# Optimization experiments

Measured on AMD Instinct MI355X. Metric: run time of the kernel, lower is better.

The kernel has to match this reference:

```python
import jax, jax.numpy as jnp
import numpy as np
import math

B = 50        # graphs per batch
NPG = 2000    # nodes per graph
EPG = 12000   # edges per graph
F_IN = 256
NHID = 128
RATIO = 0.8


def setup_inputs() -> dict:
    key = jax.random.key(0)
    ks = jax.random.split(key, 12)
    N = B * NPG
    src_loc = jax.random.randint(ks[0], (B, EPG), 0, NPG)
    dst_loc = jax.random.randint(ks[1], (B, EPG), 0, NPG)
    off = (jnp.arange(B) * NPG)[:, None]
    edge_index = jnp.stack([(src_loc + off).reshape(-1), (dst_loc + off).reshape(-1)]).astype(jnp.int32)

    def lin(k, fi, fo):
        return (jax.random.normal(k, (fi, fo), jnp.float32) / np.sqrt(fi).astype(np.float32))

    return {
        "x": jax.random.normal(ks[2], (N, F_IN), jnp.float32),
        "W1": lin(ks[3], F_IN, NHID), "b1": jnp.zeros(NHID, jnp.float32),
        "Ws1": lin(ks[4], NHID, 1), "bs1": jnp.zeros(1, jnp.float32),
        "W2": lin(ks[5], NHID, NHID), "b2": jnp.zeros(NHID, jnp.float32),
        "Ws2": lin(ks[6], NHID, 1), "bs2": jnp.zeros(1, jnp.float32),
        "W3": lin(ks[7], NHID, NHID), "b3": jnp.zeros(NHID, jnp.float32),
        "Ws3": lin(ks[8], NHID, 1), "bs3": jnp.zeros(1, jnp.float32),
        "Wl": lin(ks[9], 2 * NHID, NHID), "bl": jnp.zeros(NHID, jnp.float32),
        "edge_index": edge_index,
    }


def gcn_conv(x, W, b, src, dst, w, N):
    # PyG GCNConv: D^{-1/2} (A + I) D^{-1/2} X W + b, deg from edge weights + self loop
    h = x @ W
    deg = jax.ops.segment_sum(w, dst, num_segments=N) + 1.0
    dis = jax.lax.rsqrt(deg)
    norm = w * dis[src] * dis[dst]                       # [E]
    agg = jax.ops.segment_sum(h[src] * norm[:, None], dst, num_segments=N)
    return agg + h / deg[:, None] + b                    # self-loop norm = 1/deg


def sag_pool(x, src, dst, w, Ws, bs, n_per_graph):
    N = x.shape[0]
    k = math.ceil(RATIO * n_per_graph)
    score = gcn_conv(x, Ws, bs, src, dst, w, N)[:, 0]    # [N]
    _, topi = jax.lax.top_k(score.reshape(B, n_per_graph), k)
    perm = (topi + (jnp.arange(B) * n_per_graph)[:, None]).reshape(-1)
    x_new = x[perm] * jnp.tanh(score[perm])[:, None]
    # filter_adj: keep edges whose endpoints survive, reindex; dropped edges -> weight 0
    mapping = jnp.full((N,), -1, jnp.int32).at[perm].set(jnp.arange(B * k, dtype=jnp.int32))
    ns, nd = mapping[src], mapping[dst]
    valid = (ns >= 0) & (nd >= 0) & (w > 0)
    return (x_new, jnp.where(valid, ns, 0), jnp.where(valid, nd, 0),
            jnp.where(valid, w, jnp.zeros((), x.dtype)), k)


def readout(x, n):
    # global max pool || global mean pool (equal-size graphs, nodes grouped per graph)
    xr = x.reshape(B, n, -1)
    return jnp.concatenate([xr.max(axis=1), xr.mean(axis=1)], axis=-1)


def reference(x, W1, b1, Ws1, bs1, W2, b2, Ws2, bs2, W3, b3, Ws3, bs3, Wl, bl, edge_index):
    src, dst = edge_index[0], edge_index[1]
    w = jnp.ones(src.shape[0], x.dtype)
    n = NPG
    x = jax.nn.relu(gcn_conv(x, W1, b1, src, dst, w, B * n))
    x, src, dst, w, n = sag_pool(x, src, dst, w, Ws1, bs1, n)
    x1 = readout(x, n)
    x = jax.nn.relu(gcn_conv(x, W2, b2, src, dst, w, B * n))
    x, src, dst, w, n = sag_pool(x, src, dst, w, Ws2, bs2, n)
    x2 = readout(x, n)
    x = jax.nn.relu(gcn_conv(x, W3, b3, src, dst, w, B * n))
    x, src, dst, w, n = sag_pool(x, src, dst, w, Ws3, bs3, n)
    x3 = readout(x, n)
    return jax.nn.relu((x1 + x2 + x3) @ Wl + bl)
```

## Files before the change

kernel.cpp:

```cpp
#include <hip/hip_runtime.h>
#include <math.h>

#define B_GRAPHS 50
#define NPG0     2000
#define EPG      12000
#define F_IN_C   256
#define NHID     128
#define N0       (B_GRAPHS * NPG0)
#define NE       (B_GRAPHS * EPG)
#define RSEG     32
#define GSLOTS   7
#define CPAD     136
#define KMAX     1600

typedef _Float16 f16x8 __attribute__((ext_vector_type(8)));
typedef float    f32x4 __attribute__((ext_vector_type(4)));

static inline int cdiv(int a, int b) { return (a + b - 1) / b; }

__global__ void k_fill_start(int* __restrict__ cnt, float* __restrict__ accum) {
    int i = blockIdx.x * 256 + threadIdx.x;
    if (i < N0) cnt[i] = 0;
    if (i < B_GRAPHS * 256) accum[i] = 0.f;
}

__global__ void k_init_cvt(const int* __restrict__ ei, int* __restrict__ esrc,
                           int* __restrict__ edst, float* __restrict__ ew,
                           int* __restrict__ cnt,
                           const float* __restrict__ W1, const float* __restrict__ W2,
                           const float* __restrict__ W3, _Float16* __restrict__ WT1,
                           _Float16* __restrict__ WT2, _Float16* __restrict__ WT3) {
    int t = blockIdx.x * 256 + threadIdx.x;
    if (t < NE) {
        int d = ei[NE + t];
        esrc[t] = ei[t]; edst[t] = d; ew[t] = 1.0f;
        atomicAdd(&cnt[d], 1);
    }
    if (t < 128 * 256) {
        int n = t >> 8, kk = t & 255;
        WT1[t] = (_Float16)W1[kk * 128 + n];
    } else if (t < 128 * 256 + 128 * 128) {
        int u = t - 32768; int n = u >> 7, kk = u & 127;
        WT2[u] = (_Float16)W2[kk * 128 + n];
    } else if (t < 128 * 256 + 2 * 128 * 128) {
        int u = t - 49152; int n = u >> 7, kk = u & 127;
        WT3[u] = (_Float16)W3[kk * 128 + n];
    }
}

template<int FP32IN, int F, int GATHER>
__global__ __launch_bounds__(256) void k_gemm_ws(const void* __restrict__ Xin,
                                                 const _Float16* __restrict__ WT,
                                                 const int* __restrict__ perm,
                                                 const float* __restrict__ gate,
                                                 _Float16* __restrict__ H, int N) {
    constexpr int KH  = (F > 128) ? 128 : F;
    constexpr int K8H = KH / 8;
    constexpr int SMEMSZ = (128 * KH > 64 * CPAD) ? 128 * KH : 64 * CPAD;
    __shared__ _Float16 smem[SMEMSZ];
    const int tid  = threadIdx.x;
    const int wave = tid >> 6, lane = tid & 63;
    const int quad = lane >> 4, l16 = lane & 15;
    const int m_blk = blockIdx.x * 64;

    f32x4 acc[8];
#pragma unroll
    for (int j = 0; j < 8; ++j) acc[j] = {0.f, 0.f, 0.f, 0.f};

    int row0 = m_blk + wave * 16 + l16;
    if (row0 > N - 1) row0 = N - 1;
    _Float16 g0 = (_Float16)1.0f;
    if (GATHER) {
        g0 = (_Float16)gate[row0];
        row0 = perm[row0];
    }
    const int sx = l16 & 7;
    constexpr int NKQ = F / 32;

    if (FP32IN) {
        constexpr int PD = (NKQ < 4) ? NKQ : 4;
        const float* base0 = (const float*)Xin + (size_t)row0 * F + quad * 8;
        float4 p0[PD][2];
#pragma unroll
        for (int i = 0; i < PD; ++i) {
            p0[i][0] = ((const float4*)(base0 + i * 32))[0];
            p0[i][1] = ((const float4*)(base0 + i * 32))[1];
        }
#pragma unroll
        for (int c = tid; c < 128 * K8H; c += 256) {
            int n = c / K8H, k8 = c - n * K8H;
            f16x8 v = *(const f16x8*)&WT[(size_t)(n * (F / 8) + k8) * 8];
            *(f16x8*)&smem[n * KH + ((k8 ^ (n & 7)) << 3)] = v;
        }
        __syncthreads();
#pragma unroll
        for (int kq = 0; kq < NKQ; ++kq) {
            if (KH < F && kq == NKQ / 2) {
                __syncthreads();
#pragma unroll
                for (int c = tid; c < 128 * K8H; c += 256) {
                    int n = c / K8H, k8 = c - n * K8H;
                    f16x8 v = *(const f16x8*)&WT[(size_t)(n * (F / 8) + K8H + k8) * 8];
                    *(f16x8*)&smem[n * KH + ((k8 ^ (n & 7)) << 3)] = v;
                }
                __syncthreads();
            }
            const int b = kq % PD;
            float4 f0 = p0[b][0], f1 = p0[b][1];
            if (kq + PD < NKQ) {
                p0[b][0] = ((const float4*)(base0 + (kq + PD) * 32))[0];
                p0[b][1] = ((const float4*)(base0 + (kq + PD) * 32))[1];
            }
            f16x8 af0 = (f16x8){(_Float16)f0.x,(_Float16)f0.y,(_Float16)f0.z,(_Float16)f0.w,
                                (_Float16)f1.x,(_Float16)f1.y,(_Float16)f1.z,(_Float16)f1.w};
            f16x8 bf[8];
#pragma unroll
            for (int j = 0; j < 8; ++j)
                bf[j] = *(const f16x8*)&smem[(j * 16 + l16) * KH + (((((kq & 3) << 2) + quad) ^ sx) << 3)];
#pragma unroll
            for (int j = 0; j < 8; ++j)
                acc[j] = __builtin_amdgcn_mfma_f32_16x16x32_f16(af0, bf[j], acc[j], 0, 0, 0);
        }
    } else {
#pragma unroll
        for (int c = tid; c < 128 * K8H; c += 256) {
            int n = c / K8H, k8 = c - n * K8H;
            f16x8 v = *(const f16x8*)&WT[(size_t)(n * K8H + k8) * 8];
            *(f16x8*)&smem[n * KH + ((k8 ^ (n & 7)) << 3)] = v;
        }
        const _Float16* base0 = (const _Float16*)Xin + (size_t)row0 * F + quad * 8;
        f16x8 q0[NKQ];
#pragma unroll
        for (int i = 0; i < NKQ; ++i)
            q0[i] = *(const f16x8*)(base0 + i * 32);
        __syncthreads();
#pragma unroll
        for (int kq = 0; kq < NKQ; ++kq) {
            f16x8 af0 = q0[kq];
            if (GATHER) af0 = af0 * g0;
            f16x8 bf[8];
#pragma unroll
            for (int j = 0; j < 8; ++j)
                bf[j] = *(const f16x8*)&smem[(j * 16 + l16) * KH + (((((kq & 3) << 2) + quad) ^ sx) << 3)];
#pragma unroll
            for (int j = 0; j < 8; ++j)
                acc[j] = __builtin_amdgcn_mfma_f32_16x16x32_f16(af0, bf[j], acc[j], 0, 0, 0);
        }
    }
    __syncthreads();

    _Float16* sC = smem;
    const int rw = wave * 16;
#pragma unroll
    for (int j = 0; j < 8; ++j)
#pragma unroll
        for (int g = 0; g < 4; ++g)
            sC[(rw + quad * 4 + g) * CPAD + j * 16 + l16] = (_Float16)acc[j][g];
    __syncthreads();
    {
        int rr = tid >> 2;
        int cc = (tid & 3) * 32;
        int gr = m_blk + rr;
        if (gr < N) {
            _Float16* Hr = H + (size_t)gr * 128 + cc;
            const _Float16* Sr = sC + rr * CPAD + cc;
#pragma unroll
            for (int c = 0; c < 4; ++c)
                *(f16x8*)&Hr[c * 8] = *(const f16x8*)&Sr[c * 8];
        }
    }
}

__global__ __launch_bounds__(1024) void k_scancsr(const int* __restrict__ cnt,
                                                  int* __restrict__ offs,
                                                  const int* __restrict__ esrc,
                                                  const int* __restrict__ edst,
                                                  const float* __restrict__ ew,
                                                  int* __restrict__ csr_src,
                                                  float* __restrict__ csr_norm,
                                                  int npg) {
    __shared__ int ch[1024];
    __shared__ int scnt[2048];
    __shared__ int scur[2048];
    int b = blockIdx.x, tid = threadIdx.x;
    int base = b * npg;
    int per = (npg + 1023) >> 10;
    int s0 = tid * per;
    int s1 = s0 + per; if (s1 > npg) s1 = npg; if (s0 > npg) s0 = npg;
    int s = 0;
    for (int i = s0; i < s1; ++i) { int c = cnt[base + i]; scnt[i] = c; s += c; }
    ch[tid] = s;
    __syncthreads();
    for (int d = 1; d < 1024; d <<= 1) {
        int t = ch[tid] + ((tid >= d) ? ch[tid - d] : 0);
        __syncthreads();
        ch[tid] = t;
        __syncthreads();
    }
    int run = b * EPG + ch[tid] - s;
    for (int i = s0; i < s1; ++i) {
        offs[base + i] = run; scur[i] = run;
        run += scnt[i];
    }
    __syncthreads();
    int e0 = b * EPG;
    for (int e = tid; e < EPG; e += 1024) {
        float w = ew[e0 + e];
        if (w > 0.f) {
            int sN = esrc[e0 + e], d = edst[e0 + e];
            int pos = atomicAdd(&scur[d - base], 1);
            csr_src[pos] = sN;
            csr_norm[pos] = rsqrtf((float)(scnt[sN - base] + 1)) *
                            rsqrtf((float)(scnt[d - base] + 1));
        }
    }
}

__global__ __launch_bounds__(256) void k_agg(const _Float16* __restrict__ H,
                                             const int* __restrict__ csr_src,
                                             const float* __restrict__ csr_norm,
                                             const int* __restrict__ offs,
                                             const int* __restrict__ cnt,
                                             const float* __restrict__ bias,
                                             const float* __restrict__ Ws,
                                             _Float16* __restrict__ X,
                                             float* __restrict__ hs,
                                             int bpg, int npg) {
    int bi = blockIdx.x;
    int x = bi & 7, s = bi >> 3;
    int gslot = s / bpg, blk = s - gslot * bpg;
    int g = x + 8 * gslot;
    if (g >= B_GRAPHS) return;
    int node = g * npg + blk * 4 + (threadIdx.x >> 6);
    int lane = threadIdx.x & 63;
    int quad = lane >> 4, l16 = lane & 15;

    int st = offs[node], c = cnt[node], en = st + c;
    float acc[8];
#pragma unroll
    for (int j = 0; j < 8; ++j) acc[j] = 0.f;

    if (c > 0) {
        for (int e0 = st; e0 < en; e0 += 8) {
            int eA = e0 + quad, eB = eA + 4;
            int ecA = eA < en ? eA : en - 1;
            int ecB = eB < en ? eB : en - 1;
            int uA = csr_src[ecA], uB = csr_src[ecB];
            float nA = (eA < en) ? csr_norm[ecA] : 0.f;
            float nB = (eB < en) ? csr_norm[ecB] : 0.f;
            f16x8 hA = *(const f16x8*)&H[(size_t)uA * NHID + l16 * 8];
            f16x8 hB = *(const f16x8*)&H[(size_t)uB * NHID + l16 * 8];
#pragma unroll
            for (int j = 0; j < 8; ++j) acc[j] = fmaf((float)hA[j], nA, acc[j]);
#pragma unroll
            for (int j = 0; j < 8; ++j) acc[j] = fmaf((float)hB[j], nB, acc[j]);
        }
    }
#pragma unroll
    for (int j = 0; j < 8; ++j) {
        acc[j] += __shfl_xor(acc[j], 16, 64);
        acc[j] += __shfl_xor(acc[j], 32, 64);
    }
    float invd = 1.f / (float)(c + 1);
    f16x8 hn = *(const f16x8*)&H[(size_t)node * NHID + l16 * 8];
    float4 b0 = *(const float4*)&bias[l16 * 8];
    float4 b1 = *(const float4*)&bias[l16 * 8 + 4];
    float4 w0 = *(const float4*)&Ws[l16 * 8];
    float4 w1 = *(const float4*)&Ws[l16 * 8 + 4];
    const float bb[8] = {b0.x, b0.y, b0.z, b0.w, b1.x, b1.y, b1.z, b1.w};
    const float ww[8] = {w0.x, w0.y, w0.z, w0.w, w1.x, w1.y, w1.z, w1.w};
    float sd = 0.f;
    f16x8 o;
#pragma unroll
    for (int j = 0; j < 8; ++j) {
        float v = fmaxf(acc[j] + (float)hn[j] * invd + bb[j], 0.f);
        o[j] = (_Float16)v;
        sd = fmaf(v, ww[j], sd);
    }
    if (quad == 0)
        *(f16x8*)&X[(size_t)node * NHID + l16 * 8] = o;
    sd += __shfl_xor(sd, 1, 64);
    sd += __shfl_xor(sd, 2, 64);
    sd += __shfl_xor(sd, 4, 64);
    sd += __shfl_xor(sd, 8, 64);
    if (lane == 0) hs[node] = sd;
}

template<int REMAP, int COMB>
__global__ __launch_bounds__(1024) void k_scoretopk(const float* __restrict__ hs,
                                                    int* __restrict__ csr_src,
                                                    float* __restrict__ csr_norm,
                                                    int* __restrict__ offs,
                                                    const int* __restrict__ cnt,
                                                    const float* __restrict__ bs,
                                                    int* __restrict__ perm,
                                                    float* __restrict__ gate,
                                                    int* __restrict__ esrc,
                                                    int* __restrict__ edst,
                                                    float* __restrict__ ew,
                                                    int* __restrict__ cntN,
                                                    const float* __restrict__ pmax,
                                                    const float* __restrict__ psum,
                                                    float* __restrict__ accum,
                                                    int npg, int k) {
    __shared__ float ss[2048];
    __shared__ int   si[2048];
    __shared__ float shs[2048];
    __shared__ int   shist[KMAX];
    int b = blockIdx.x, tid = threadIdx.x;
    int base = b * npg;

    if (COMB) {
        if (tid < 2 * NHID) {
            int f = tid & 127;
            bool isSum = tid >= NHID;
            float a2 = isSum ? 0.f : -__builtin_inff();
            for (int s = 0; s < RSEG; ++s) {
                float v = (isSum ? psum : pmax)[(size_t)(b * RSEG + s) * NHID + f];
                a2 = isSum ? (a2 + v) : fmaxf(a2, v);
            }
            if (isSum) accum[b * 256 + 128 + f] += a2 / (float)npg;
            else       accum[b * 256 + f]       += a2;
        }
    }

    float bs0 = bs[0];
    for (int i = tid; i < 2048; i += 1024)
        shs[i] = (i < npg) ? hs[base + i] : 0.f;
    __syncthreads();
    for (int i = tid; i < 2048; i += 1024) {
        if (i < npg) {
            int st = offs[base + i], c = cnt[base + i];
            float a = 0.f;
            for (int e = st; e < st + c; ++e)
                a = fmaf(shs[csr_src[e] - base], csr_norm[e], a);
            ss[i] = a + shs[i] / (float)(c + 1) + bs0;
        } else {
            ss[i] = -__builtin_inff();
        }
        si[i] = i;
    }
    __syncthreads();
    for (int size = 2; size <= 2048; size <<= 1) {
        for (int stride = size >> 1; stride > 0; stride >>= 1) {
            int t = tid;
            int i = ((t & ~(stride - 1)) << 1) | (t & (stride - 1));
            int j = i | stride;
            float sa = ss[i], sb = ss[j];
            int   ia = si[i], ib = si[j];
            bool b_before_a = (sb > sa) || (sb == sa && ib < ia);
            bool forward = ((i & size) == 0);
            bool doswap = forward ? b_before_a : !b_before_a;
            if (doswap) { ss[i] = sb; ss[j] = sa; si[i] = ib; si[j] = ia; }
            __syncthreads();
        }
    }
    int* smap = (int*)shs;
    for (int j = tid; j < npg; j += 1024) {
        int ol = si[j];
        if (j < k) {
            int newg = b * k + j;
            perm[newg] = base + ol;
            smap[ol] = newg;
            gate[newg] = tanhf(ss[j]);
        } else {
            smap[ol] = -1;
        }
    }
    if (REMAP) {
        for (int j = tid; j < k; j += 1024) shist[j] = 0;
        __syncthreads();
        int e0 = b * EPG;
        for (int e = tid; e < EPG; e += 1024) {
            int idx = e0 + e;
            float w = ew[idx];
            bool valid = false;
            int ns = 0, nd = 0;
            if (w > 0.f) {
                ns = smap[esrc[idx] - base];
                nd = smap[edst[idx] - base];
                valid = (ns >= 0) && (nd >= 0);
            }
            esrc[idx] = valid ? ns : 0;
            edst[idx] = valid ? nd : 0;
            ew[idx]   = valid ? w : 0.f;
            if (valid) atomicAdd(&shist[nd - b * k], 1);
        }
        __syncthreads();
        int* sscan = (int*)ss;
        int* scur  = si;
        int per2 = (k + 1023) >> 10;
        int t0 = tid * per2, t1 = t0 + per2;
        if (t1 > k) t1 = k; if (t0 > k) t0 = k;
        int sloc = 0;
        for (int i = t0; i < t1; ++i) sloc += shist[i];
        sscan[tid] = sloc;
        __syncthreads();
        for (int d = 1; d < 1024; d <<= 1) {
            int t = sscan[tid] + ((tid >= d) ? sscan[tid - d] : 0);
            __syncthreads();
            sscan[tid] = t;
            __syncthreads();
        }
        int run = b * EPG + sscan[tid] - sloc;
        for (int i = t0; i < t1; ++i) {
            offs[b * k + i] = run; scur[i] = run;
            cntN[b * k + i] = shist[i];
            run += shist[i];
        }
        __syncthreads();
        for (int e = tid; e < EPG; e += 1024) {
            int idx = e0 + e;
            float w = ew[idx];
            if (w > 0.f) {
                int ns = esrc[idx], nd = edst[idx];
                int pos = atomicAdd(&scur[nd - b * k], 1);
                csr_src[pos] = ns;
                csr_norm[pos] = rsqrtf((float)(shist[ns - b * k] + 1)) *
                                rsqrtf((float)(shist[nd - b * k] + 1));
            }
        }
    }
}

__global__ __launch_bounds__(128) void k_pool_readout(const _Float16* __restrict__ X,
                                                      const float* __restrict__ gate,
                                                      const int* __restrict__ perm,
                                                      float* __restrict__ pmax,
                                                      float* __restrict__ psum, int k) {
    int s = blockIdx.x, b = blockIdx.y, f = threadIdx.x;
    int j0 = (k * s) / RSEG, j1 = (k * (s + 1)) / RSEG;
    float mx = -__builtin_inff(), sm = 0.f;
    for (int j = j0; j < j1; ++j) {
        int g = b * k + j;
        int old = perm[g];
        float v = (float)X[(size_t)old * NHID + f] * gate[g];
        mx = fmaxf(mx, v);
        sm += v;
    }
    pmax[(size_t)(b * RSEG + s) * NHID + f] = mx;
    psum[(size_t)(b * RSEG + s) * NHID + f] = sm;
}

__global__ __launch_bounds__(128) void k_comb_final(const float* __restrict__ pmax,
                                                    const float* __restrict__ psum,
                                                    const float* __restrict__ accum,
                                                    const float* __restrict__ Wl,
                                                    const float* __restrict__ bl,
                                                    float* __restrict__ out, int k) {
    __shared__ float a[256];
    int b = blockIdx.x, f = threadIdx.x;
    float mx = -__builtin_inff(), sm = 0.f;
#pragma unroll
    for (int s = 0; s < RSEG; ++s) {
        mx = fmaxf(mx, pmax[(size_t)(b * RSEG + s) * NHID + f]);
        sm += psum[(size_t)(b * RSEG + s) * NHID + f];
    }
    a[f]       = accum[b * 256 + f] + mx;
    a[128 + f] = accum[b * 256 + 128 + f] + sm / (float)k;
    __syncthreads();
    float s = bl[f];
    for (int i = 0; i < 256; ++i) s = fmaf(a[i], Wl[i * NHID + f], s);
    out[b * NHID + f] = fmaxf(s, 0.f);
}

extern "C" void kernel_launch(void* const* d_in, const int* in_sizes, int n_in,
                              void* d_out, int out_size, void* d_ws, size_t ws_size,
                              hipStream_t stream) {
    const float* x0 = (const float*)d_in[0];
    const float* Wm[3] = {(const float*)d_in[1], (const float*)d_in[5], (const float*)d_in[9]};
    const float* bm[3] = {(const float*)d_in[2], (const float*)d_in[6], (const float*)d_in[10]};
    const float* Wsc[3] = {(const float*)d_in[3], (const float*)d_in[7], (const float*)d_in[11]};
    const float* bsc[3] = {(const float*)d_in[4], (const float*)d_in[8], (const float*)d_in[12]};
    const float* Wl = (const float*)d_in[13];
    const float* bl = (const float*)d_in[14];
    const int*   ei = (const int*)d_in[15];
    float* out = (float*)d_out;

    _Float16* bufA = (_Float16*)d_ws;
    _Float16* bufB = bufA + (size_t)N0 * NHID;
    _Float16* WT1  = bufB + (size_t)N0 * NHID;
    _Float16* WT2  = WT1 + 128 * 256;
    _Float16* WT3  = WT2 + 128 * 128;
    float* hs     = (float*)(WT3 + 128 * 128);
    float* gate   = hs + N0;
    float* accum  = gate + N0;
    float* pmax   = accum + B_GRAPHS * 256;
    float* psum   = pmax + B_GRAPHS * RSEG * NHID;
    int*   cntA   = (int*)(psum + B_GRAPHS * RSEG * NHID);
    int*   cntB   = cntA + N0;
    int*   offs   = cntB + N0;
    int*   perm   = offs + N0;
    int*   esrc   = perm + N0;
    int*   edst   = esrc + NE;
    float* ew     = (float*)(edst + NE);
    int*   csr_src= (int*)(ew + NE);
    float* csr_norm = (float*)(csr_src + NE);

    _Float16* WTs[3] = {WT1, WT2, WT3};
    const int EG = cdiv(NE, 256);

    k_fill_start<<<cdiv(N0, 256), 256, 0, stream>>>(cntA, accum);
    k_init_cvt<<<EG, 256, 0, stream>>>(ei, esrc, edst, ew, cntA,
                                       Wm[0], Wm[1], Wm[2], WT1, WT2, WT3);

    int npg = NPG0;
    _Float16* Hbuf = bufA; _Float16* Xbuf = bufB;

    for (int layer = 0; layer < 3; ++layer) {
        int N = B_GRAPHS * npg;
        int k = (npg * 4) / 5;
        int bpg = npg >> 2;
        int* cnt  = (layer == 1) ? cntB : cntA;
        int* cntN = (layer == 1) ? cntA : cntB;

        if (layer == 0) {
            k_gemm_ws<1, 256, 0><<<cdiv(N, 64), 256, 0, stream>>>(x0, WTs[0], perm, gate, Hbuf, N);
            k_scancsr<<<B_GRAPHS, 1024, 0, stream>>>(cnt, offs, esrc, edst, ew,
                                                     csr_src, csr_norm, npg);
        } else {
            k_gemm_ws<0, 128, 1><<<cdiv(N, 64), 256, 0, stream>>>(Xbuf, WTs[layer], perm, gate, Hbuf, N);
        }
        k_agg<<<8 * GSLOTS * bpg, 256, 0, stream>>>(Hbuf, csr_src, csr_norm, offs, cnt,
                                                    bm[layer], Wsc[layer], Xbuf, hs, bpg, npg);
        if (layer == 0)
            k_scoretopk<1, 0><<<B_GRAPHS, 1024, 0, stream>>>(hs, csr_src, csr_norm, offs, cnt,
                                                             bsc[layer], perm, gate,
                                                             esrc, edst, ew, cntN,
                                                             pmax, psum, accum, npg, k);
        else if (layer == 1)
            k_scoretopk<1, 1><<<B_GRAPHS, 1024, 0, stream>>>(hs, csr_src, csr_norm, offs, cnt,
                                                             bsc[layer], perm, gate,
                                                             esrc, edst, ew, cntN,
                                                             pmax, psum, accum, npg, k);
        else
            k_scoretopk<0, 1><<<B_GRAPHS, 1024, 0, stream>>>(hs, csr_src, csr_norm, offs, cnt,
                                                             bsc[layer], perm, gate,
                                                             esrc, edst, ew, cntN,
                                                             pmax, psum, accum, npg, k);
        k_pool_readout<<<dim3(RSEG, B_GRAPHS), 128, 0, stream>>>(Xbuf, gate, perm, pmax, psum, k);
        if (layer == 2)
            k_comb_final<<<B_GRAPHS, 128, 0, stream>>>(pmax, psum, accum, Wl, bl, out, k);

        npg = k;
    }
}
```

Baseline: 549.6 us.

## Do bitonic sort strides up to 64 in registers with wave shuffles

The block-wide bitonic top-k sort over 2048 scores used shared memory plus a __syncthreads for every compare-exchange step. Now each 64-lane wave keeps 128 contiguous elements in registers and performs strides of 64 and below with __shfl_xor and in-register swaps, falling back to shared memory and barriers only for strides of 128 and above. This removes most block barriers and LDS traffic in the pooling kernel, at the cost of extra register use and more complex index logic.

```diff
diff --git a/kernel.cpp b/kernel.cpp
--- a/kernel.cpp
+++ b/kernel.cpp
@@ -341,20 +341,65 @@
         si[i] = i;
     }
     __syncthreads();
-    for (int size = 2; size <= 2048; size <<= 1) {
-        for (int stride = size >> 1; stride > 0; stride >>= 1) {
-            int t = tid;
-            int i = ((t & ~(stride - 1)) << 1) | (t & (stride - 1));
+
+    const int wbase = (tid >> 6) << 7;
+    const int l = tid & 63;
+    float vL = ss[wbase + l],      vH = ss[wbase + 64 + l];
+    int   iL = si[wbase + l],      iH = si[wbase + 64 + l];
+
+    auto reg_steps = [&](int size, int smax) {
+        for (int s = smax; s > 0; s >>= 1) {
+            if (s == 64) {
+                bool fwd = (((wbase + l) & size) == 0);
+                bool bba = (vH > vL) || (vH == vL && iH < iL);
+                if (fwd ? bba : !bba) {
+                    float tv = vL; vL = vH; vH = tv;
+                    int ti = iL; iL = iH; iH = ti;
+                }
+            } else {
+                bool iR = ((l & s) == 0);
+                float pv = __shfl_xor(vL, s, 64);
+                int   pi = __shfl_xor(iL, s, 64);
+                float sa = iR ? vL : pv, sb = iR ? pv : vL;
+                int   ia = iR ? iL : pi, ib = iR ? pi : iL;
+                bool bba = (sb > sa) || (sb == sa && ib < ia);
+                bool fwd = (((wbase + l) & size) == 0);
+                if (fwd ? bba : !bba) { vL = pv; iL = pi; }
+                pv = __shfl_xor(vH, s, 64);
+                pi = __shfl_xor(iH, s, 64);
+                sa = iR ? vH : pv; sb = iR ? pv : vH;
+                ia = iR ? iH : pi; ib = iR ? pi : iH;
+                bba = (sb > sa) || (sb == sa && ib < ia);
+                bool fwd2 = (((wbase + 64 + l) & size) == 0);
+                if (fwd2 ? bba : !bba) { vH = pv; iH = pi; }
+            }
+        }
+    };
+
+    for (int size = 2; size <= 128; size <<= 1)
+        reg_steps(size, size >> 1);
+    for (int size = 256; size <= 2048; size <<= 1) {
+        ss[wbase + l] = vL;      si[wbase + l] = iL;
+        ss[wbase + 64 + l] = vH; si[wbase + 64 + l] = iH;
+        __syncthreads();
+        for (int stride = size >> 1; stride >= 128; stride >>= 1) {
+            int i = ((tid & ~(stride - 1)) << 1) | (tid & (stride - 1));
             int j = i | stride;
             float sa = ss[i], sb = ss[j];
             int   ia = si[i], ib = si[j];
-            bool b_before_a = (sb > sa) || (sb == sa && ib < ia);
-            bool forward = ((i & size) == 0);
-            bool doswap = forward ? b_before_a : !b_before_a;
-            if (doswap) { ss[i] = sb; ss[j] = sa; si[i] = ib; si[j] = ia; }
+            bool bba = (sb > sa) || (sb == sa && ib < ia);
+            bool fwd = ((i & size) == 0);
+            if (fwd ? bba : !bba) { ss[i] = sb; ss[j] = sa; si[i] = ib; si[j] = ia; }
             __syncthreads();
         }
-    }
+        vL = ss[wbase + l];      iL = si[wbase + l];
+        vH = ss[wbase + 64 + l]; iH = si[wbase + 64 + l];
+        reg_steps(size, 64);
+    }
+    ss[wbase + l] = vL;      si[wbase + l] = iL;
+    ss[wbase + 64 + l] = vH; si[wbase + 64 + l] = iH;
+    __syncthreads();
+
     int* smap = (int*)shs;
     for (int j = tid; j < npg; j += 1024) {
         int ol = si[j];
```

After: 543.4 us. About the same (-1.1%).
